# Kernel tuning notes

Measured on AMD Instinct MI355X. Metric: run time of the kernel, lower is better.

## Reference

```python
import jax, jax.numpy as jnp
import numpy as np

B = 1024
IN_SHAPE = ((8, 8, 8), (8, 8))
IN_RANKS = ((32, 32, 32), (32, 32))
OUT_SHAPE = (16, 16, 16)
OUT_RANK = (32, 32, 32)


def _xavier(key, shape):
    # xavier_normal over axes [0,1] (in) and [2] (out), matching the torch helper
    fan_in = shape[0] * shape[1]
    fan_out = shape[2]
    std = float(np.sqrt(2.0 / (fan_in + fan_out)))
    return jax.random.normal(key, shape, dtype=jnp.float32) * std


def setup_inputs() -> dict:
    key = jax.random.key(0)
    ks = jax.random.split(key, 12)
    x_dims = tuple(d for g in IN_SHAPE for d in g)
    inp = {"x": jax.random.normal(ks[0], (B,) + x_dims, dtype=jnp.float32)}
    # input TT factors, flattened over groups in order (group, mode)
    fac_shapes = []
    for shapes, ranks in zip(IN_SHAPE, IN_RANKS):
        for i in range(len(shapes)):
            r_prev = 1 if i == 0 else ranks[i - 1]
            fac_shapes.append((r_prev, shapes[i], ranks[i]))
    for idx, fs in enumerate(fac_shapes):
        inp[f"f{idx}"] = _xavier(ks[1 + idx], fs)
    # core: (last rank of each group..., output_rank[-1])
    core_shape = tuple(r[-1] for r in IN_RANKS) + (OUT_RANK[-1],)
    fan_in = int(np.prod(core_shape[:-1]))
    std = float(np.sqrt(2.0 / (fan_in + core_shape[-1])))
    inp["core"] = jax.random.normal(ks[6], core_shape, dtype=jnp.float32) * std
    # output TT factors
    for i in range(len(OUT_SHAPE)):
        r_prev = 1 if i == 0 else OUT_RANK[i - 1]
        inp[f"g{i}"] = _xavier(ks[7 + i], (r_prev, OUT_SHAPE[i], OUT_RANK[i]))
    # bias: uniform(-1/sqrt(fan_in), +) with fan_in = total input features
    total_in = int(np.prod([np.prod(s) for s in IN_SHAPE]))
    bound = 1.0 / float(np.sqrt(total_in))
    inp["bias"] = jax.random.uniform(ks[10], OUT_SHAPE, dtype=jnp.float32,
                                     minval=-bound, maxval=bound)
    return inp


def reference(x, f0, f1, f2, f3, f4, core, g0, g1, g2, bias):
    groups = ((f0, f1, f2), (f3, f4))
    Bsz = x.shape[0]
    # T: [B, remaining_modes_flat, accumulated_group_ranks_flat]
    T = x.reshape(Bsz, -1)[:, :, None]
    for facs in groups:
        first = facs[0][0]                       # squeeze dummy rank-1: [n, r]
        n = first.shape[0]
        T = T.reshape(Bsz, n, -1, T.shape[-1])   # [B, n, M', Racc]
        T = jnp.einsum("bnmq,nr->bmqr", T, first)  # [B, M', Racc, r]
        for f in facs[1:]:
            n = f.shape[1]
            T = T.reshape(Bsz, n, -1, T.shape[-2], T.shape[-1])
            T = jnp.einsum("bnmqp,pnr->bmqr", T, f)
        # fold this group's final rank into the accumulated rank axis
        T = T.reshape(Bsz, T.shape[1], -1)
    # all input modes consumed -> T is [B, 1, r1_last*r2_last]
    z = T.reshape(Bsz, -1) @ core.reshape(-1, core.shape[-1])  # [B, Rout]
    # output TT chain -> W[o0, o1, o2, R_last]
    W = g0[0]
    for g in (g1, g2):
        W = jnp.einsum("...p,poq->...oq", W, g)
    R = W.shape[-1]
    out = z @ W.reshape(-1, R).T                 # [B, prod(OUT_SHAPE)]
    out = out.reshape((Bsz,) + OUT_SHAPE)
    return out + bias
```

## Files before the change

kernel.cpp:

```cpp
#include <hip/hip_runtime.h>

#define WS_M2 0
#define WS_N2 16384
#define WS_WT 18432
#define WS_Z  149504

__global__ __launch_bounds__(256) void precompute_kernel(
    const float* __restrict__ f0, const float* __restrict__ f1,
    const float* __restrict__ f2, const float* __restrict__ f3,
    const float* __restrict__ f4, const float* __restrict__ g0,
    const float* __restrict__ g1, const float* __restrict__ g2,
    float* __restrict__ ws)
{
    __shared__ float sA[8192];
    const int t = threadIdx.x;
    const int blk = blockIdx.x;
    if (blk < 8) {
        for (int i = t; i < 2048; i += 256) {
            int a01 = i >> 5, r2 = i & 31;
            int a0 = a01 >> 3, a1 = a01 & 7;
            float s = 0.f;
            #pragma unroll
            for (int r1 = 0; r1 < 32; ++r1)
                s += f0[a0*32 + r1] * f1[r1*256 + a1*32 + r2];
            sA[i] = s;
        }
        __syncthreads();
        for (int i = t; i < 2048; i += 256) {
            int a012 = blk*64 + (i >> 5), r3 = i & 31;
            int a01 = a012 >> 3, a2 = a012 & 7;
            float s = 0.f;
            #pragma unroll
            for (int r2 = 0; r2 < 32; ++r2)
                s += sA[a01*32 + r2] * f2[r2*256 + a2*32 + r3];
            ws[WS_M2 + a012*32 + r3] = s;
        }
    } else if (blk == 8) {
        for (int i = t; i < 2048; i += 256) {
            int a34 = i >> 5, s2 = i & 31;
            int a3 = a34 >> 3, a4 = a34 & 7;
            float s = 0.f;
            #pragma unroll
            for (int s1 = 0; s1 < 32; ++s1)
                s += f3[a3*32 + s1] * f4[s1*256 + a4*32 + s2];
            ws[WS_N2 + i] = s;
        }
    } else {
        const int j = blk - 9;
        for (int i = t; i < 8192; i += 256) {
            int o01 = i >> 5, q = i & 31;
            int o0 = o01 >> 4, o1 = o01 & 15;
            float s = 0.f;
            #pragma unroll
            for (int p = 0; p < 32; ++p)
                s += g0[o0*32 + p] * g1[p*512 + o1*32 + q];
            sA[i] = s;
        }
        __syncthreads();
        for (int i = t; i < 4096; i += 256) {
            int o = j*128 + (i >> 5);
            int r = i & 31;
            int o01 = o >> 4, o2 = o & 15;
            float s = 0.f;
            #pragma unroll
            for (int q = 0; q < 32; ++q)
                s += sA[o01*32 + q] * g2[q*512 + o2*32 + r];
            ws[WS_WT + r*4096 + o] = s;
        }
    }
}

__global__ __launch_bounds__(256) void main_kernel(
    const float* __restrict__ x, const float* __restrict__ core,
    const float* __restrict__ ws, float* __restrict__ zout)
{
    __shared__ float sx[4096];
    __shared__ float sM[2048];
    __shared__ float sN[2048];
    const int t = threadIdx.x;
    const int b = blockIdx.x;

    float4* sx4 = (float4*)sx;
    float4* sM4 = (float4*)sM;

    {
        const float4* n24 = (const float4*)(ws + WS_N2);
        float4* d = (float4*)sN;
        d[t]       = n24[t];
        d[256 + t] = n24[256 + t];
    }

    const int m4 = t & 15;
    const int rg = t >> 4;
    float acc[4][2] = {{0.f,0.f},{0.f,0.f},{0.f,0.f},{0.f,0.f}};
    const float4* x4 = (const float4*)(x + (size_t)b * 32768);
    const float4* m24 = (const float4*)(ws + WS_M2);

    for (int c = 0; c < 8; ++c) {
        const float4* xs = x4 + c*1024;
        #pragma unroll
        for (int i = 0; i < 4; ++i) sx4[i*256 + t] = xs[i*256 + t];
        const float4* ms = m24 + c*512;
        #pragma unroll
        for (int i = 0; i < 2; ++i) sM4[i*256 + t] = ms[i*256 + t];
        __syncthreads();

        #pragma unroll 16
        for (int k = 0; k < 64; ++k) {
            float4 xv = sx4[k*16 + m4];
            float2 wv = *(const float2*)&sM[k*32 + rg*2];
            acc[0][0] += xv.x * wv.x; acc[0][1] += xv.x * wv.y;
            acc[1][0] += xv.y * wv.x; acc[1][1] += xv.y * wv.y;
            acc[2][0] += xv.z * wv.x; acc[2][1] += xv.z * wv.y;
            acc[3][0] += xv.w * wv.x; acc[3][1] += xv.w * wv.y;
        }
        __syncthreads();
    }

    #pragma unroll
    for (int j = 0; j < 4; ++j) {
        sx[(m4*4 + j)*33 + rg*2 + 0] = acc[j][0];
        sx[(m4*4 + j)*33 + rg*2 + 1] = acc[j][1];
    }
    __syncthreads();

    {
        const int r3  = t >> 3;
        const int s2b = (t & 7) * 4;
        float a0=0.f, a1=0.f, a2=0.f, a3=0.f;
        #pragma unroll 8
        for (int m = 0; m < 64; ++m) {
            float av = sx[m*33 + r3];
            const float* n = &sN[m*32 + s2b];
            a0 += av * n[0]; a1 += av * n[1]; a2 += av * n[2]; a3 += av * n[3];
        }
        float* d = &sM[r3*32 + s2b];
        d[0]=a0; d[1]=a1; d[2]=a2; d[3]=a3;
    }
    __syncthreads();

    {
        const int ro2 = t & 15;
        const int kc  = t >> 4;
        const float2* core2 = (const float2*)core;
        float s0 = 0.f, s1 = 0.f;
        const int k0 = kc * 64;
        for (int k = k0; k < k0 + 64; ++k) {
            float tv = sM[k];
            float2 cv = core2[k*16 + ro2];
            s0 += tv * cv.x; s1 += tv * cv.y;
        }
        sM[1024 + kc*32 + ro2*2 + 0] = s0;
        sM[1024 + kc*32 + ro2*2 + 1] = s1;
    }
    __syncthreads();
    if (t < 32) {
        float s = 0.f;
        #pragma unroll
        for (int kc = 0; kc < 16; ++kc) s += sM[1024 + kc*32 + t];
        zout[b*32 + t] = s;
    }
}

__global__ __launch_bounds__(256) void out_kernel(
    const float* __restrict__ ws, const float* __restrict__ bias,
    float* __restrict__ out)
{
    __shared__ float sW[8192];
    __shared__ float sZt[2176];
    __shared__ float sB[256];
    const int t  = threadIdx.x;
    const int bt = blockIdx.x;
    const int ot = blockIdx.y;

    {
        const float4* wt4 = (const float4*)(ws + WS_WT);
        float4* d = (float4*)sW;
        #pragma unroll
        for (int i = 0; i < 8; ++i) {
            int idx = i*256 + t;
            int ro = idx >> 6, oc = idx & 63;
            d[idx] = wt4[ro*1024 + ot*64 + oc];
        }
    }
    {
        const float4* z4 = (const float4*)(ws + WS_Z) + bt*512;
        #pragma unroll
        for (int i = 0; i < 2; ++i) {
            int idx = i*256 + t;
            int bl = idx >> 3, r4 = idx & 7;
            float4 v = z4[idx];
            sZt[(r4*4 + 0)*68 + bl] = v.x;
            sZt[(r4*4 + 1)*68 + bl] = v.y;
            sZt[(r4*4 + 2)*68 + bl] = v.z;
            sZt[(r4*4 + 3)*68 + bl] = v.w;
        }
    }
    if (t < 64) {
        const float4* b4 = (const float4*)bias + ot*64;
        ((float4*)sB)[t] = b4[t];
    }
    __syncthreads();

    const int oc = t & 63;
    const int bg = t >> 6;
    const float4* sW4 = (const float4*)sW;
    const float4 bv = ((const float4*)sB)[oc];
    float4* out4 = (float4*)out;

    for (int bi = 0; bi < 16; bi += 4) {
        const int bl = bg*16 + bi;
        float4 a0 = bv, a1 = bv, a2 = bv, a3 = bv;
        #pragma unroll
        for (int ro = 0; ro < 32; ++ro) {
            float4 w = sW4[ro*64 + oc];
            float4 z = *(const float4*)&sZt[ro*68 + bl];
            a0.x += z.x*w.x; a0.y += z.x*w.y; a0.z += z.x*w.z; a0.w += z.x*w.w;
            a1.x += z.y*w.x; a1.y += z.y*w.y; a1.z += z.y*w.z; a1.w += z.y*w.w;
            a2.x += z.z*w.x; a2.y += z.z*w.y; a2.z += z.z*w.z; a2.w += z.z*w.w;
            a3.x += z.w*w.x; a3.y += z.w*w.y; a3.z += z.w*w.z; a3.w += z.w*w.w;
        }
        const size_t obase = (size_t)(bt*64 + bl) * 1024 + ot*64 + oc;
        out4[obase + 0*1024] = a0;
        out4[obase + 1*1024] = a1;
        out4[obase + 2*1024] = a2;
        out4[obase + 3*1024] = a3;
    }
}

extern "C" void kernel_launch(void* const* d_in, const int* in_sizes, int n_in,
                              void* d_out, int out_size, void* d_ws, size_t ws_size,
                              hipStream_t stream)
{
    const float* x    = (const float*)d_in[0];
    const float* f0   = (const float*)d_in[1];
    const float* f1   = (const float*)d_in[2];
    const float* f2   = (const float*)d_in[3];
    const float* f3   = (const float*)d_in[4];
    const float* f4   = (const float*)d_in[5];
    const float* core = (const float*)d_in[6];
    const float* g0   = (const float*)d_in[7];
    const float* g1   = (const float*)d_in[8];
    const float* g2   = (const float*)d_in[9];
    const float* bias = (const float*)d_in[10];
    float* ws  = (float*)d_ws;
    float* out = (float*)d_out;

    precompute_kernel<<<41, 256, 0, stream>>>(f0, f1, f2, f3, f4, g0, g1, g2, ws);
    main_kernel<<<1024, 256, 0, stream>>>(x, core, ws, ws + WS_Z);
    out_kernel<<<dim3(16, 16), 256, 0, stream>>>(ws, bias, out);
}
```

Measured before the change: 268.0 us.

## Retile main kernel first contraction with 8x4 register blocking and split-K reduction

Restructures the first per-batch contraction in main_kernel so each thread computes an 8x4 output tile over a quarter of the k range, instead of a 4x2 tile over the full range. The four partial results are then summed through shared memory. Shared memory is consolidated into one reused buffer, with the N2 factor load moved after the first stage, and launch bounds now request 4 blocks per SM. This raises arithmetic intensity per shared-memory load and improves occupancy, at the cost of more registers per thread and an extra reduction pass with its syncs.

```diff
diff --git a/kernel.cpp b/kernel.cpp
--- a/kernel.cpp
+++ b/kernel.cpp
@@ -70,57 +70,74 @@
     }
 }
 
-__global__ __launch_bounds__(256) void main_kernel(
+__global__ __launch_bounds__(256, 4) void main_kernel(
     const float* __restrict__ x, const float* __restrict__ core,
     const float* __restrict__ ws, float* __restrict__ zout)
 {
-    __shared__ float sx[4096];
-    __shared__ float sM[2048];
-    __shared__ float sN[2048];
+    __shared__ float buf[8192];
+    __shared__ float spart[512];
     const int t = threadIdx.x;
     const int b = blockIdx.x;
 
-    float4* sx4 = (float4*)sx;
-    float4* sM4 = (float4*)sM;
-
-    {
-        const float4* n24 = (const float4*)(ws + WS_N2);
-        float4* d = (float4*)sN;
-        d[t]       = n24[t];
-        d[256 + t] = n24[256 + t];
-    }
-
-    const int m4 = t & 15;
-    const int rg = t >> 4;
-    float acc[4][2] = {{0.f,0.f},{0.f,0.f},{0.f,0.f},{0.f,0.f}};
-    const float4* x4 = (const float4*)(x + (size_t)b * 32768);
+    const int tk = t >> 6;
+    const int tm = (t >> 3) & 7;
+    const int tr = t & 7;
+
+    float4* buf4 = (float4*)buf;
+    const float4* x4  = (const float4*)(x + (size_t)b * 32768);
     const float4* m24 = (const float4*)(ws + WS_M2);
+
+    float acc[8][4];
+    #pragma unroll
+    for (int i = 0; i < 8; ++i)
+        #pragma unroll
+        for (int j = 0; j < 4; ++j) acc[i][j] = 0.f;
 
     for (int c = 0; c < 8; ++c) {
         const float4* xs = x4 + c*1024;
         #pragma unroll
-        for (int i = 0; i < 4; ++i) sx4[i*256 + t] = xs[i*256 + t];
+        for (int i = 0; i < 4; ++i) buf4[i*256 + t] = xs[i*256 + t];
         const float4* ms = m24 + c*512;
         #pragma unroll
-        for (int i = 0; i < 2; ++i) sM4[i*256 + t] = ms[i*256 + t];
-        __syncthreads();
-
-        #pragma unroll 16
-        for (int k = 0; k < 64; ++k) {
-            float4 xv = sx4[k*16 + m4];
-            float2 wv = *(const float2*)&sM[k*32 + rg*2];
-            acc[0][0] += xv.x * wv.x; acc[0][1] += xv.x * wv.y;
-            acc[1][0] += xv.y * wv.x; acc[1][1] += xv.y * wv.y;
-            acc[2][0] += xv.z * wv.x; acc[2][1] += xv.z * wv.y;
-            acc[3][0] += xv.w * wv.x; acc[3][1] += xv.w * wv.y;
+        for (int i = 0; i < 2; ++i) buf4[1024 + i*256 + t] = ms[i*256 + t];
+        __syncthreads();
+
+        #pragma unroll 4
+        for (int k0 = 0; k0 < 16; ++k0) {
+            const int k = tk*16 + k0;
+            float4 xa = buf4[k*16 + tm*2];
+            float4 xb = buf4[k*16 + tm*2 + 1];
+            float4 wv = buf4[1024 + k*8 + tr];
+            const float xm[8] = {xa.x,xa.y,xa.z,xa.w, xb.x,xb.y,xb.z,xb.w};
+            #pragma unroll
+            for (int i = 0; i < 8; ++i) {
+                acc[i][0] += xm[i]*wv.x; acc[i][1] += xm[i]*wv.y;
+                acc[i][2] += xm[i]*wv.z; acc[i][3] += xm[i]*wv.w;
+            }
         }
         __syncthreads();
     }
 
     #pragma unroll
-    for (int j = 0; j < 4; ++j) {
-        sx[(m4*4 + j)*33 + rg*2 + 0] = acc[j][0];
-        sx[(m4*4 + j)*33 + rg*2 + 1] = acc[j][1];
+    for (int i = 0; i < 8; ++i) {
+        float4 v = {acc[i][0], acc[i][1], acc[i][2], acc[i][3]};
+        buf4[tk*512 + (tm*8 + i)*8 + tr] = v;
+    }
+    __syncthreads();
+
+    {
+        float4 s0 = buf4[t*2], s1 = buf4[t*2 + 1];
+        #pragma unroll
+        for (int q = 1; q < 4; ++q) {
+            float4 a = buf4[q*512 + t*2], c2 = buf4[q*512 + t*2 + 1];
+            s0.x+=a.x; s0.y+=a.y; s0.z+=a.z; s0.w+=a.w;
+            s1.x+=c2.x; s1.y+=c2.y; s1.z+=c2.z; s1.w+=c2.w;
+        }
+        __syncthreads();
+        buf4[t*2] = s0; buf4[t*2 + 1] = s1;
+        const float4* n24 = (const float4*)(ws + WS_N2);
+        buf4[512 + t] = n24[t];
+        buf4[768 + t] = n24[256 + t];
     }
     __syncthreads();
 
@@ -130,11 +147,11 @@
         float a0=0.f, a1=0.f, a2=0.f, a3=0.f;
         #pragma unroll 8
         for (int m = 0; m < 64; ++m) {
-            float av = sx[m*33 + r3];
-            const float* n = &sN[m*32 + s2b];
-            a0 += av * n[0]; a1 += av * n[1]; a2 += av * n[2]; a3 += av * n[3];
-        }
-        float* d = &sM[r3*32 + s2b];
+            float av = buf[m*32 + r3];
+            const float* n = &buf[2048 + m*32 + s2b];
+            a0 += av*n[0]; a1 += av*n[1]; a2 += av*n[2]; a3 += av*n[3];
+        }
+        float* d = &buf[4096 + r3*32 + s2b];
         d[0]=a0; d[1]=a1; d[2]=a2; d[3]=a3;
     }
     __syncthreads();
@@ -146,18 +163,18 @@
         float s0 = 0.f, s1 = 0.f;
         const int k0 = kc * 64;
         for (int k = k0; k < k0 + 64; ++k) {
-            float tv = sM[k];
+            float tv = buf[4096 + k];
             float2 cv = core2[k*16 + ro2];
-            s0 += tv * cv.x; s1 += tv * cv.y;
-        }
-        sM[1024 + kc*32 + ro2*2 + 0] = s0;
-        sM[1024 + kc*32 + ro2*2 + 1] = s1;
+            s0 += tv*cv.x; s1 += tv*cv.y;
+        }
+        spart[kc*32 + ro2*2 + 0] = s0;
+        spart[kc*32 + ro2*2 + 1] = s1;
     }
     __syncthreads();
     if (t < 32) {
         float s = 0.f;
         #pragma unroll
-        for (int kc = 0; kc < 16; ++kc) s += sM[1024 + kc*32 + t];
+        for (int kc = 0; kc < 16; ++kc) s += spart[kc*32 + t];
         zout[b*32 + t] = s;
     }
 }
```

Result: no change. 266.4 us (-0.6%).
